# Performance work log

Hardware: AMD Instinct MI355X
Metric: run time of the kernel (lower is better)

Reference implementation:

```python
import jax, jax.numpy as jnp
import numpy as np

N_NODES = 50000
N_EDGES = 800000
NUM_HEADS = 4
HEAD_DIM = 32
IN_DIM = 128
NEG_SLOPE = 0.2


def setup_inputs() -> dict:
    key = jax.random.key(0)
    k1, k2, k3, k4, k5, k6 = jax.random.split(key, 6)
    x = jax.random.normal(k1, (N_NODES, IN_DIM), dtype=jnp.float32)
    W = jax.random.normal(k2, (NUM_HEADS * HEAD_DIM, IN_DIM), dtype=jnp.float32) * 0.05
    attn_l = jax.random.normal(k3, (NUM_HEADS, HEAD_DIM), dtype=jnp.float32) * 0.05
    attn_r = jax.random.normal(k4, (NUM_HEADS, HEAD_DIM), dtype=jnp.float32) * 0.05
    src = jax.random.randint(k5, (N_EDGES,), 0, N_NODES, dtype=jnp.int32)
    dst = jnp.sort(jax.random.randint(k6, (N_EDGES,), 0, N_NODES, dtype=jnp.int32))
    return {"x": x, "W": W, "attn_l": attn_l, "attn_r": attn_r, "src": src, "dst": dst}


def reference(x, W, attn_l, attn_r, src, dst):
    N = x.shape[0]
    H, D = attn_l.shape
    # linear projection: [N, H*D] -> [N, H, D]
    feat = (x @ W.T).reshape(N, H, D)
    # per-node attention terms  [N, H]
    el = jnp.einsum('nhd,hd->nh', feat, attn_l)
    er = jnp.einsum('nhd,hd->nh', feat, attn_r)
    # per-edge logits (u_add_v) + leaky relu  [E, H]
    e = el[src] + er[dst]
    e = jnp.where(e > 0, e, NEG_SLOPE * e)
    # edge softmax segmented by destination node
    e_max = jax.ops.segment_max(e, dst, num_segments=N)          # [N, H]
    e_exp = jnp.exp(e - e_max[dst])                              # [E, H]
    denom = jax.ops.segment_sum(e_exp, dst, num_segments=N)     # [N, H]
    alpha = e_exp / denom[dst]                                   # [E, H]
    # attention-weighted neighbor aggregation  [N, H, D]
    out = jax.ops.segment_sum(alpha[:, :, None] * feat[src], dst, num_segments=N)
    return out.reshape(N, H * D)
```

## Files before the change

### kernel.cpp

```cpp
#include <hip/hip_runtime.h>
#include <math.h>

#define NN 50000
#define NE 800000
#define NH 4
#define HD 32
#define FD 128
#define NTILE 3125

typedef __attribute__((ext_vector_type(8))) short short8;
typedef __attribute__((ext_vector_type(4))) float floatx4;

__device__ __forceinline__ unsigned short f2bf(float f) {
    union { float f; unsigned u; } v; v.f = f;
    unsigned u = v.u;
    return (unsigned short)((u + 0x7FFFu + ((u >> 16) & 1u)) >> 16);
}
__device__ __forceinline__ float bf_lo(unsigned u) {
    union { unsigned u; float f; } v; v.u = u << 16; return v.f;
}
__device__ __forceinline__ float bf_hi(unsigned u) {
    union { unsigned u; float f; } v; v.u = u & 0xFFFF0000u; return v.f;
}

__global__ __launch_bounds__(256) void k_gemm_mfma(const float* __restrict__ x,
                                                   const float* __restrict__ W,
                                                   unsigned short* __restrict__ feat_bf) {
    __shared__ unsigned short Wl[FD * 136];
    const int tid = threadIdx.x;

    for (int p = tid; p < FD * 64; p += 256) {
        int c = p >> 6, k2 = (p & 63) * 2;
        float2 wv = *(const float2*)&W[c * FD + k2];
        unsigned lo = f2bf(wv.x), hi = f2bf(wv.y);
        *(unsigned*)&Wl[c * 136 + k2] = lo | (hi << 16);
    }
    __syncthreads();

    const int wv_id = tid >> 6, lane = tid & 63;
    const int col = lane & 15, quad = lane >> 4;
    const int tile = blockIdx.x * 4 + wv_id;
    if (tile >= NTILE) return;
    const int n0 = tile * 16;

    short8 afrag[4];
    const float* xrow = x + (size_t)(n0 + col) * FD;
    #pragma unroll
    for (int s = 0; s < 4; ++s) {
        float4 u0 = *(const float4*)&xrow[s * 32 + quad * 8];
        float4 u1 = *(const float4*)&xrow[s * 32 + quad * 8 + 4];
        short8 a;
        a[0] = (short)f2bf(u0.x); a[1] = (short)f2bf(u0.y);
        a[2] = (short)f2bf(u0.z); a[3] = (short)f2bf(u0.w);
        a[4] = (short)f2bf(u1.x); a[5] = (short)f2bf(u1.y);
        a[6] = (short)f2bf(u1.z); a[7] = (short)f2bf(u1.w);
        afrag[s] = a;
    }

    floatx4 acc[8];
    #pragma unroll
    for (int ct = 0; ct < 8; ++ct) acc[ct] = (floatx4){0.f, 0.f, 0.f, 0.f};

    #pragma unroll
    for (int ct = 0; ct < 8; ++ct) {
        #pragma unroll
        for (int s = 0; s < 4; ++s) {
            short8 b = *(const short8*)&Wl[(ct * 16 + col) * 136 + s * 32 + quad * 8];
            acc[ct] = __builtin_amdgcn_mfma_f32_16x16x32_bf16(afrag[s], b, acc[ct], 0, 0, 0);
        }
    }

    #pragma unroll
    for (int ct = 0; ct < 8; ++ct) {
        #pragma unroll
        for (int r = 0; r < 4; ++r) {
            int n = n0 + quad * 4 + r;
            feat_bf[(size_t)n * FD + ct * 16 + col] = f2bf(acc[ct][r]);
        }
    }
}

__global__ void k_nodeattn(const unsigned short* __restrict__ feat_bf,
                           const float* __restrict__ al,
                           const float* __restrict__ ar,
                           float* __restrict__ el,
                           float* __restrict__ er) {
    int i = blockIdx.x * blockDim.x + threadIdx.x;
    if (i >= NN * NH) return;
    int h = i & 3;
    const uint4* f = (const uint4*)(feat_bf + (size_t)i * HD);
    const float* a = al + h * HD;
    const float* b = ar + h * HD;
    float sl = 0.f, sr = 0.f;
    #pragma unroll
    for (int j = 0; j < 4; ++j) {
        uint4 u = f[j];
        float fv[8] = {bf_lo(u.x), bf_hi(u.x), bf_lo(u.y), bf_hi(u.y),
                       bf_lo(u.z), bf_hi(u.z), bf_lo(u.w), bf_hi(u.w)};
        #pragma unroll
        for (int t = 0; t < 8; ++t) {
            sl += fv[t] * a[j * 8 + t];
            sr += fv[t] * b[j * 8 + t];
        }
    }
    el[i] = sl;
    er[i] = sr;
}

__global__ void k_rows(const int* __restrict__ dst, int* __restrict__ rows) {
    int i = blockIdx.x * blockDim.x + threadIdx.x;
    if (i >= NE) return;
    int cur = dst[i];
    if (i == 0) {
        for (int n = 0; n <= cur; ++n) rows[n] = 0;
    } else {
        int prev = dst[i - 1];
        for (int n = prev + 1; n <= cur; ++n) rows[n] = i;
    }
    if (i == NE - 1) {
        for (int n = cur + 1; n <= NN; ++n) rows[n] = NE;
    }
}

__global__ void k_edgew(const float* __restrict__ el,
                        const float* __restrict__ er,
                        const int* __restrict__ src,
                        const int* __restrict__ dst,
                        float* __restrict__ wT) {
    int e = blockIdx.x * blockDim.x + threadIdx.x;
    if (e >= NE) return;
    int sj = src[e], dj = dst[e];
    float4 el4 = *(const float4*)&el[sj * NH];
    float4 er4 = *(const float4*)&er[dj * NH];
    float lg, z;
    lg = el4.x + er4.x; z = fmaxf(lg, 0.2f * lg); wT[0 * NE + e] = __expf(z);
    lg = el4.y + er4.y; z = fmaxf(lg, 0.2f * lg); wT[1 * NE + e] = __expf(z);
    lg = el4.z + er4.z; z = fmaxf(lg, 0.2f * lg); wT[2 * NE + e] = __expf(z);
    lg = el4.w + er4.w; z = fmaxf(lg, 0.2f * lg); wT[3 * NE + e] = __expf(z);
}

__global__ __launch_bounds__(256) void k_aggregate(const unsigned short* __restrict__ feat_bf,
                                                   const float* __restrict__ wT,
                                                   const int* __restrict__ src,
                                                   const int* __restrict__ rows,
                                                   float* __restrict__ out) {
    const int wave = threadIdx.x >> 6;
    const int lane = threadIdx.x & 63;
    const int n = blockIdx.x * 4 + wave;
    if (n >= NN) return;

    const int s = rows[n], t = rows[n + 1];
    const int h = lane >> 4;
    const float* wh = wT + (size_t)h * NE;

    float2 acc = make_float2(0.f, 0.f);
    float den = 0.f;

    int e = s;
    for (; e + 4 <= t; e += 4) {
        int sj0 = src[e], sj1 = src[e + 1], sj2 = src[e + 2], sj3 = src[e + 3];
        float w0 = wh[e], w1 = wh[e + 1], w2 = wh[e + 2], w3 = wh[e + 3];
        unsigned u0 = *(const unsigned*)&feat_bf[(size_t)sj0 * FD + 2 * lane];
        unsigned u1 = *(const unsigned*)&feat_bf[(size_t)sj1 * FD + 2 * lane];
        unsigned u2 = *(const unsigned*)&feat_bf[(size_t)sj2 * FD + 2 * lane];
        unsigned u3 = *(const unsigned*)&feat_bf[(size_t)sj3 * FD + 2 * lane];
        acc.x += w0 * bf_lo(u0) + w1 * bf_lo(u1) + w2 * bf_lo(u2) + w3 * bf_lo(u3);
        acc.y += w0 * bf_hi(u0) + w1 * bf_hi(u1) + w2 * bf_hi(u2) + w3 * bf_hi(u3);
        den   += (w0 + w1) + (w2 + w3);
    }
    for (; e < t; ++e) {
        int sj = src[e];
        float w = wh[e];
        unsigned u = *(const unsigned*)&feat_bf[(size_t)sj * FD + 2 * lane];
        acc.x += w * bf_lo(u);
        acc.y += w * bf_hi(u);
        den   += w;
    }

    const float rden = (den > 0.f) ? 1.f / den : 0.f;
    *(float2*)&out[(size_t)n * FD + 2 * lane] = make_float2(acc.x * rden, acc.y * rden);
}

extern "C" void kernel_launch(void* const* d_in, const int* in_sizes, int n_in,
                              void* d_out, int out_size, void* d_ws, size_t ws_size,
                              hipStream_t stream) {
    const float* x  = (const float*)d_in[0];
    const float* W  = (const float*)d_in[1];
    const float* al = (const float*)d_in[2];
    const float* ar = (const float*)d_in[3];
    const int* src  = (const int*)d_in[4];
    const int* dst  = (const int*)d_in[5];
    float* out = (float*)d_out;

    unsigned short* feat_bf = (unsigned short*)d_ws;
    float* el = (float*)(feat_bf + (size_t)NN * FD);
    float* er = el + (size_t)NN * NH;
    int*   rows = (int*)(er + (size_t)NN * NH);
    float* wT = (float*)(rows + (NN + 1) + 3);

    k_gemm_mfma<<<(NTILE + 3) / 4, 256, 0, stream>>>(x, W, feat_bf);
    k_nodeattn<<<(NN * NH + 255) / 256, 256, 0, stream>>>(feat_bf, al, ar, el, er);
    k_rows<<<(NE + 255) / 256, 256, 0, stream>>>(dst, rows);
    k_edgew<<<(NE + 255) / 256, 256, 0, stream>>>(el, er, src, dst, wT);
    k_aggregate<<<(NN + 3) / 4, 256, 0, stream>>>(feat_bf, wT, src, rows, out);
}
```

Baseline: 150.0 us.

## Fuse node attention into GEMM, rows into edge kernel, and widen aggregate loads

The per-node attention dot products now come from the MFMA accumulators inside a persistent GEMM kernel using cross-lane shuffles, so the separate pass that re-read feat_bf is gone. The CSR row-offset build is folded into the edge-weight kernel, and edge weights are stored edge-major as float4 instead of head-major. The aggregate kernel now has each quarter-wave handle a different edge with 16-byte feature loads, then reduces across quarters with shuffles. This cuts kernel launches and memory traffic and increases load width, at the cost of extra shuffle work and predicated tail handling.

```diff
diff --git a/kernel.cpp b/kernel.cpp
--- a/kernel.cpp
+++ b/kernel.cpp
@@ -23,102 +23,91 @@
     union { unsigned u; float f; } v; v.u = u & 0xFFFF0000u; return v.f;
 }
 
-__global__ __launch_bounds__(256) void k_gemm_mfma(const float* __restrict__ x,
-                                                   const float* __restrict__ W,
-                                                   unsigned short* __restrict__ feat_bf) {
+__global__ __launch_bounds__(512) void k_gemm_fused(const float* __restrict__ x,
+                                                    const float* __restrict__ W,
+                                                    const float* __restrict__ al,
+                                                    const float* __restrict__ ar,
+                                                    unsigned short* __restrict__ feat_bf,
+                                                    float* __restrict__ el,
+                                                    float* __restrict__ er) {
     __shared__ unsigned short Wl[FD * 136];
     const int tid = threadIdx.x;
 
-    for (int p = tid; p < FD * 64; p += 256) {
+    for (int p = tid; p < FD * 64; p += 512) {
         int c = p >> 6, k2 = (p & 63) * 2;
         float2 wv = *(const float2*)&W[c * FD + k2];
-        unsigned lo = f2bf(wv.x), hi = f2bf(wv.y);
-        *(unsigned*)&Wl[c * 136 + k2] = lo | (hi << 16);
+        *(unsigned*)&Wl[c * 136 + k2] =
+            (unsigned)f2bf(wv.x) | ((unsigned)f2bf(wv.y) << 16);
     }
     __syncthreads();
 
     const int wv_id = tid >> 6, lane = tid & 63;
     const int col = lane & 15, quad = lane >> 4;
-    const int tile = blockIdx.x * 4 + wv_id;
-    if (tile >= NTILE) return;
-    const int n0 = tile * 16;
-
-    short8 afrag[4];
-    const float* xrow = x + (size_t)(n0 + col) * FD;
-    #pragma unroll
-    for (int s = 0; s < 4; ++s) {
-        float4 u0 = *(const float4*)&xrow[s * 32 + quad * 8];
-        float4 u1 = *(const float4*)&xrow[s * 32 + quad * 8 + 4];
-        short8 a;
-        a[0] = (short)f2bf(u0.x); a[1] = (short)f2bf(u0.y);
-        a[2] = (short)f2bf(u0.z); a[3] = (short)f2bf(u0.w);
-        a[4] = (short)f2bf(u1.x); a[5] = (short)f2bf(u1.y);
-        a[6] = (short)f2bf(u1.z); a[7] = (short)f2bf(u1.w);
-        afrag[s] = a;
-    }
-
-    floatx4 acc[8];
-    #pragma unroll
-    for (int ct = 0; ct < 8; ++ct) acc[ct] = (floatx4){0.f, 0.f, 0.f, 0.f};
-
+
+    float alr[8], arr[8];
     #pragma unroll
     for (int ct = 0; ct < 8; ++ct) {
+        alr[ct] = al[col + 16 * ct];
+        arr[ct] = ar[col + 16 * ct];
+    }
+
+    for (int tile = blockIdx.x * 8 + wv_id; tile < NTILE; tile += gridDim.x * 8) {
+        const int n0 = tile * 16;
+
+        short8 afrag[4];
+        const float* xrow = x + (size_t)(n0 + col) * FD;
         #pragma unroll
         for (int s = 0; s < 4; ++s) {
-            short8 b = *(const short8*)&Wl[(ct * 16 + col) * 136 + s * 32 + quad * 8];
-            acc[ct] = __builtin_amdgcn_mfma_f32_16x16x32_bf16(afrag[s], b, acc[ct], 0, 0, 0);
-        }
-    }
-
-    #pragma unroll
-    for (int ct = 0; ct < 8; ++ct) {
+            float4 u0 = *(const float4*)&xrow[s * 32 + quad * 8];
+            float4 u1 = *(const float4*)&xrow[s * 32 + quad * 8 + 4];
+            short8 a;
+            a[0] = (short)f2bf(u0.x); a[1] = (short)f2bf(u0.y);
+            a[2] = (short)f2bf(u0.z); a[3] = (short)f2bf(u0.w);
+            a[4] = (short)f2bf(u1.x); a[5] = (short)f2bf(u1.y);
+            a[6] = (short)f2bf(u1.z); a[7] = (short)f2bf(u1.w);
+            afrag[s] = a;
+        }
+
+        floatx4 acc[8];
+        #pragma unroll
+        for (int ct = 0; ct < 8; ++ct) acc[ct] = (floatx4){0.f, 0.f, 0.f, 0.f};
+
+        #pragma unroll
+        for (int ct = 0; ct < 8; ++ct) {
+            #pragma unroll
+            for (int s = 0; s < 4; ++s) {
+                short8 b = *(const short8*)&Wl[(ct * 16 + col) * 136 + s * 32 + quad * 8];
+                acc[ct] = __builtin_amdgcn_mfma_f32_16x16x32_bf16(afrag[s], b, acc[ct], 0, 0, 0);
+            }
+        }
+
+        #pragma unroll
+        for (int ct = 0; ct < 8; ++ct) {
+            #pragma unroll
+            for (int r = 0; r < 4; ++r) {
+                feat_bf[(size_t)(n0 + quad * 4 + r) * FD + ct * 16 + col] = f2bf(acc[ct][r]);
+            }
+        }
+
         #pragma unroll
         for (int r = 0; r < 4; ++r) {
-            int n = n0 + quad * 4 + r;
-            feat_bf[(size_t)n * FD + ct * 16 + col] = f2bf(acc[ct][r]);
-        }
-    }
-}
-
-__global__ void k_nodeattn(const unsigned short* __restrict__ feat_bf,
-                           const float* __restrict__ al,
-                           const float* __restrict__ ar,
-                           float* __restrict__ el,
-                           float* __restrict__ er) {
-    int i = blockIdx.x * blockDim.x + threadIdx.x;
-    if (i >= NN * NH) return;
-    int h = i & 3;
-    const uint4* f = (const uint4*)(feat_bf + (size_t)i * HD);
-    const float* a = al + h * HD;
-    const float* b = ar + h * HD;
-    float sl = 0.f, sr = 0.f;
-    #pragma unroll
-    for (int j = 0; j < 4; ++j) {
-        uint4 u = f[j];
-        float fv[8] = {bf_lo(u.x), bf_hi(u.x), bf_lo(u.y), bf_hi(u.y),
-                       bf_lo(u.z), bf_hi(u.z), bf_lo(u.w), bf_hi(u.w)};
-        #pragma unroll
-        for (int t = 0; t < 8; ++t) {
-            sl += fv[t] * a[j * 8 + t];
-            sr += fv[t] * b[j * 8 + t];
-        }
-    }
-    el[i] = sl;
-    er[i] = sr;
-}
-
-__global__ void k_rows(const int* __restrict__ dst, int* __restrict__ rows) {
-    int i = blockIdx.x * blockDim.x + threadIdx.x;
-    if (i >= NE) return;
-    int cur = dst[i];
-    if (i == 0) {
-        for (int n = 0; n <= cur; ++n) rows[n] = 0;
-    } else {
-        int prev = dst[i - 1];
-        for (int n = prev + 1; n <= cur; ++n) rows[n] = i;
-    }
-    if (i == NE - 1) {
-        for (int n = cur + 1; n <= NN; ++n) rows[n] = NE;
+            float ev[8];
+            #pragma unroll
+            for (int hh = 0; hh < NH; ++hh) {
+                ev[hh]     = acc[2 * hh][r] * alr[2 * hh] + acc[2 * hh + 1][r] * alr[2 * hh + 1];
+                ev[4 + hh] = acc[2 * hh][r] * arr[2 * hh] + acc[2 * hh + 1][r] * arr[2 * hh + 1];
+            }
+            #pragma unroll
+            for (int m = 1; m < 16; m <<= 1) {
+                #pragma unroll
+                for (int j = 0; j < 8; ++j) ev[j] += __shfl_xor(ev[j], m);
+            }
+            if (col == 0) {
+                int n = n0 + quad * 4 + r;
+                *(float4*)&el[n * NH] = make_float4(ev[0], ev[1], ev[2], ev[3]);
+                *(float4*)&er[n * NH] = make_float4(ev[4], ev[5], ev[6], ev[7]);
+            }
+        }
     }
 }
 
@@ -126,21 +115,35 @@
                         const float* __restrict__ er,
                         const int* __restrict__ src,
                         const int* __restrict__ dst,
-                        float* __restrict__ wT) {
+                        float* __restrict__ wE,
+                        int* __restrict__ rows) {
     int e = blockIdx.x * blockDim.x + threadIdx.x;
     if (e >= NE) return;
     int sj = src[e], dj = dst[e];
+
+    if (e == 0) {
+        for (int n = 0; n <= dj; ++n) rows[n] = 0;
+    } else {
+        int prev = dst[e - 1];
+        for (int n = prev + 1; n <= dj; ++n) rows[n] = e;
+    }
+    if (e == NE - 1) {
+        for (int n = dj + 1; n <= NN; ++n) rows[n] = NE;
+    }
+
     float4 el4 = *(const float4*)&el[sj * NH];
     float4 er4 = *(const float4*)&er[dj * NH];
+    float4 w;
     float lg, z;
-    lg = el4.x + er4.x; z = fmaxf(lg, 0.2f * lg); wT[0 * NE + e] = __expf(z);
-    lg = el4.y + er4.y; z = fmaxf(lg, 0.2f * lg); wT[1 * NE + e] = __expf(z);
-    lg = el4.z + er4.z; z = fmaxf(lg, 0.2f * lg); wT[2 * NE + e] = __expf(z);
-    lg = el4.w + er4.w; z = fmaxf(lg, 0.2f * lg); wT[3 * NE + e] = __expf(z);
+    lg = el4.x + er4.x; z = fmaxf(lg, 0.2f * lg); w.x = __expf(z);
+    lg = el4.y + er4.y; z = fmaxf(lg, 0.2f * lg); w.y = __expf(z);
+    lg = el4.z + er4.z; z = fmaxf(lg, 0.2f * lg); w.z = __expf(z);
+    lg = el4.w + er4.w; z = fmaxf(lg, 0.2f * lg); w.w = __expf(z);
+    *(float4*)&wE[e * NH] = w;
 }
 
 __global__ __launch_bounds__(256) void k_aggregate(const unsigned short* __restrict__ feat_bf,
-                                                   const float* __restrict__ wT,
+                                                   const float* __restrict__ wE,
                                                    const int* __restrict__ src,
                                                    const int* __restrict__ rows,
                                                    float* __restrict__ out) {
@@ -150,35 +153,53 @@
     if (n >= NN) return;
 
     const int s = rows[n], t = rows[n + 1];
-    const int h = lane >> 4;
-    const float* wh = wT + (size_t)h * NE;
-
-    float2 acc = make_float2(0.f, 0.f);
+    const int q  = lane >> 4;
+    const int lp = lane & 15;
+    const int h  = lp >> 2;
+    const int dimoff = 8 * lp;
+
+    float acc[8] = {0.f, 0.f, 0.f, 0.f, 0.f, 0.f, 0.f, 0.f};
     float den = 0.f;
 
-    int e = s;
-    for (; e + 4 <= t; e += 4) {
-        int sj0 = src[e], sj1 = src[e + 1], sj2 = src[e + 2], sj3 = src[e + 3];
-        float w0 = wh[e], w1 = wh[e + 1], w2 = wh[e + 2], w3 = wh[e + 3];
-        unsigned u0 = *(const unsigned*)&feat_bf[(size_t)sj0 * FD + 2 * lane];
-        unsigned u1 = *(const unsigned*)&feat_bf[(size_t)sj1 * FD + 2 * lane];
-        unsigned u2 = *(const unsigned*)&feat_bf[(size_t)sj2 * FD + 2 * lane];
-        unsigned u3 = *(const unsigned*)&feat_bf[(size_t)sj3 * FD + 2 * lane];
-        acc.x += w0 * bf_lo(u0) + w1 * bf_lo(u1) + w2 * bf_lo(u2) + w3 * bf_lo(u3);
-        acc.y += w0 * bf_hi(u0) + w1 * bf_hi(u1) + w2 * bf_hi(u2) + w3 * bf_hi(u3);
-        den   += (w0 + w1) + (w2 + w3);
-    }
-    for (; e < t; ++e) {
-        int sj = src[e];
-        float w = wh[e];
-        unsigned u = *(const unsigned*)&feat_bf[(size_t)sj * FD + 2 * lane];
-        acc.x += w * bf_lo(u);
-        acc.y += w * bf_hi(u);
-        den   += w;
-    }
-
-    const float rden = (den > 0.f) ? 1.f / den : 0.f;
-    *(float2*)&out[(size_t)n * FD + 2 * lane] = make_float2(acc.x * rden, acc.y * rden);
+    for (int e = s; e < t; e += 16) {
+        int   sjv[4];
+        float wv4[4];
+        #pragma unroll
+        for (int u = 0; u < 4; ++u) {
+            int ei = e + 4 * u + q;
+            int ec = (ei < t) ? ei : (t - 1);
+            sjv[u] = src[ec];
+            wv4[u] = (ei < t) ? wE[ec * NH + h] : 0.f;
+        }
+        uint4 uvv[4];
+        #pragma unroll
+        for (int u = 0; u < 4; ++u)
+            uvv[u] = *(const uint4*)&feat_bf[(size_t)sjv[u] * FD + dimoff];
+        #pragma unroll
+        for (int u = 0; u < 4; ++u) {
+            float w = wv4[u];
+            uint4 uv = uvv[u];
+            acc[0] += w * bf_lo(uv.x); acc[1] += w * bf_hi(uv.x);
+            acc[2] += w * bf_lo(uv.y); acc[3] += w * bf_hi(uv.y);
+            acc[4] += w * bf_lo(uv.z); acc[5] += w * bf_hi(uv.z);
+            acc[6] += w * bf_lo(uv.w); acc[7] += w * bf_hi(uv.w);
+            den += w;
+        }
+    }
+
+    #pragma unroll
+    for (int m = 16; m < 64; m <<= 1) {
+        #pragma unroll
+        for (int j = 0; j < 8; ++j) acc[j] += __shfl_xor(acc[j], m);
+        den += __shfl_xor(den, m);
+    }
+
+    if (q == 0) {
+        const float rden = (den > 0.f) ? 1.f / den : 0.f;
+        float* op = out + (size_t)n * FD + dimoff;
+        *(float4*)op       = make_float4(acc[0] * rden, acc[1] * rden, acc[2] * rden, acc[3] * rden);
+        *(float4*)(op + 4) = make_float4(acc[4] * rden, acc[5] * rden, acc[6] * rden, acc[7] * rden);
+    }
 }
 
 extern "C" void kernel_launch(void* const* d_in, const int* in_sizes, int n_in,
@@ -196,11 +217,9 @@
     float* el = (float*)(feat_bf + (size_t)NN * FD);
     float* er = el + (size_t)NN * NH;
     int*   rows = (int*)(er + (size_t)NN * NH);
-    float* wT = (float*)(rows + (NN + 1) + 3);
-
-    k_gemm_mfma<<<(NTILE + 3) / 4, 256, 0, stream>>>(x, W, feat_bf);
-    k_nodeattn<<<(NN * NH + 255) / 256, 256, 0, stream>>>(feat_bf, al, ar, el, er);
-    k_rows<<<(NE + 255) / 256, 256, 0, stream>>>(dst, rows);
-    k_edgew<<<(NE + 255) / 256, 256, 0, stream>>>(el, er, src, dst, wT);
-    k_aggregate<<<(NN + 3) / 4, 256, 0, stream>>>(feat_bf, wT, src, rows, out);
-}
+    float* wE = (float*)(((uintptr_t)(rows + NN + 1) + 15) & ~(uintptr_t)15);
+
+    k_gemm_fused<<<256, 512, 0, stream>>>(x, W, al, ar, feat_bf, el, er);
+    k_edgew<<<(NE + 255) / 256, 256, 0, stream>>>(el, er, src, dst, wE, rows);
+    k_aggregate<<<(NN + 3) / 4, 256, 0, stream>>>(feat_bf, wE, src, rows, out);
+}
```

New measurement: 133.6 us. -10.9%, faster.
